# Optimization experiments

Hardware: AMD Instinct MI355X
Metric: run time of the kernel (lower is better)

The kernel has to match this reference:

```python
import jax, jax.numpy as jnp
import numpy as np

B, N, H = 128, 512, 512
NEG_INF = -1e30


def setup_inputs() -> dict:
    key = jax.random.key(0)
    k1, k2, k3, k4 = jax.random.split(key, 4)
    code_feat = jax.random.normal(k1, (B, N, H), dtype=jnp.float32)
    node_mask = jax.random.randint(k2, (B, N), 0, 2, dtype=jnp.int32)
    node_mask = node_mask.at[:, 0].set(1)  # ensure >=1 valid node per sample
    scale = 1.0 / np.sqrt(H)
    W_sa = jax.random.normal(k3, (H, H), dtype=jnp.float32) * scale
    b_sa = jnp.zeros((H,), dtype=jnp.float32)
    w_sc = jax.random.normal(k4, (H,), dtype=jnp.float32) * scale
    b_sc = jnp.zeros((), dtype=jnp.float32)
    return {"code_feat": code_feat, "node_mask": node_mask,
            "W_sa": W_sa, "b_sa": b_sa, "w_sc": w_sc, "b_sc": b_sc}


def reference(code_feat, node_mask, W_sa, b_sa, w_sc, b_sc):
    # code_sa_tanh = self_atten_scalar(tanh(self_atten(code_feat)))  -> [B, N]
    h = jnp.tanh(jnp.einsum('bnh,hk->bnk', code_feat, W_sa) + b_sa)
    scores = jnp.einsum('bnk,k->bn', h, w_sc) + b_sc  # [B, N]
    valid = node_mask.astype(bool)
    # masked_select + softmax over selected nodes == masked softmax; invalid
    # positions get weight 0, so the weighted sum over all nodes matches the
    # original per-sample bmm over the ragged selection exactly.
    scores = jnp.where(valid, scores, NEG_INF)
    attn = jax.nn.softmax(scores, axis=1)  # [B, N]
    pooled = jnp.einsum('bn,bnh->bh', attn, code_feat)  # [B, H]
    return jnp.tanh(pooled)
```

## Files before the change

### kernel.cpp

```cpp
#include <hip/hip_runtime.h>

#define NEG_INF (-1e30f)

typedef __bf16 bf16x8 __attribute__((ext_vector_type(8)));
typedef float  f32x4  __attribute__((ext_vector_type(4)));
typedef unsigned short ushort;

__device__ __forceinline__ float fast_tanhf(float x) {
    return 1.0f - 2.0f / (1.0f + __expf(2.0f * x));
}

__device__ __forceinline__ ushort f2bf(float f) {
    union { float f; unsigned u; } v; v.f = f;
    unsigned r = v.u + 0x7fffu + ((v.u >> 16) & 1u);
    return (ushort)(r >> 16);
}

__device__ __forceinline__ void gload_lds16(const void* gsrc, void* ldsdst) {
    __builtin_amdgcn_global_load_lds(
        (const __attribute__((address_space(1))) unsigned int*)gsrc,
        (__attribute__((address_space(3))) unsigned int*)ldsdst, 16, 0, 0);
}

__global__ void convw_kernel(const float* __restrict__ W, ushort* __restrict__ Wt) {
    int i = blockIdx.x * 256 + threadIdx.x;
    int h = i >> 9, c = i & 511;
    Wt[c * 512 + h] = f2bf(W[i]);
}

__global__ __launch_bounds__(256) void gemm_scores_kernel(
    const float* __restrict__ feat, const ushort* __restrict__ Wt,
    const float* __restrict__ b_sa, const float* __restrict__ w_sc,
    float* __restrict__ sp) {

    __shared__ ushort Alds[128 * 40];
    __shared__ ushort Blds[128 * 32];
    __shared__ float  redE[4][64];

    const int tid  = threadIdx.x;
    const int by   = blockIdx.x;
    const int m0   = blockIdx.y * 128;
    const int n0   = by * 128;
    const int lane = tid & 63;
    const int wv   = tid >> 6;
    const int wm   = wv >> 1, wn = wv & 1;
    const int lr   = lane & 15;
    const int kg   = lane >> 4;
    const int lk   = kg * 8;

    const int arow = tid >> 1;
    const int aseg = (tid & 1) * 16;
    const float* agp = feat + (size_t)(m0 + arow) * 512 + aseg;

    f32x4 acc[4][4];
#pragma unroll
    for (int a = 0; a < 4; ++a)
#pragma unroll
        for (int b = 0; b < 4; ++b) acc[a][b] = (f32x4){0.f, 0.f, 0.f, 0.f};

    const int o1 = tid + 256;
    const ushort* bg0 = Wt + (size_t)(n0 + (tid >> 2)) * 512 + (tid & 3) * 8;
    const ushort* bg1 = Wt + (size_t)(n0 + (o1 >> 2)) * 512 + (o1 & 3) * 8;

    for (int k0 = 0; k0 < 512; k0 += 32) {
        const float4 v0 = *reinterpret_cast<const float4*>(agp + k0);
        const float4 v1 = *reinterpret_cast<const float4*>(agp + k0 + 4);
        const float4 v2 = *reinterpret_cast<const float4*>(agp + k0 + 8);
        const float4 v3 = *reinterpret_cast<const float4*>(agp + k0 + 12);

        __syncthreads();

        gload_lds16(bg0 + k0, (char*)Blds + wv * 1024);
        gload_lds16(bg1 + k0, (char*)Blds + 4096 + wv * 1024);

        bf16x8 h0, h1;
        h0[0] = (__bf16)v0.x; h0[1] = (__bf16)v0.y; h0[2] = (__bf16)v0.z; h0[3] = (__bf16)v0.w;
        h0[4] = (__bf16)v1.x; h0[5] = (__bf16)v1.y; h0[6] = (__bf16)v1.z; h0[7] = (__bf16)v1.w;
        h1[0] = (__bf16)v2.x; h1[1] = (__bf16)v2.y; h1[2] = (__bf16)v2.z; h1[3] = (__bf16)v2.w;
        h1[4] = (__bf16)v3.x; h1[5] = (__bf16)v3.y; h1[6] = (__bf16)v3.z; h1[7] = (__bf16)v3.w;
        *reinterpret_cast<bf16x8*>(&Alds[arow * 40 + aseg]) = h0;
        *reinterpret_cast<bf16x8*>(&Alds[arow * 40 + aseg + 8]) = h1;

        __syncthreads();

        bf16x8 af[4], bfv[4];
#pragma unroll
        for (int a = 0; a < 4; ++a)
            af[a] = *reinterpret_cast<const bf16x8*>(
                &Alds[(wm * 64 + a * 16 + lr) * 40 + lk]);
#pragma unroll
        for (int b = 0; b < 4; ++b)
            bfv[b] = *reinterpret_cast<const bf16x8*>(&Blds[(wn * 64 + b * 16 + lr) * 32 + lk]);
#pragma unroll
        for (int a = 0; a < 4; ++a)
#pragma unroll
            for (int b = 0; b < 4; ++b)
                acc[a][b] = __builtin_amdgcn_mfma_f32_16x16x32_bf16(
                    af[a], bfv[b], acc[a][b], 0, 0, 0);
    }

    float rsum[4][4];
#pragma unroll
    for (int a = 0; a < 4; ++a)
#pragma unroll
        for (int r = 0; r < 4; ++r) rsum[a][r] = 0.0f;

#pragma unroll
    for (int b = 0; b < 4; ++b) {
        int col = n0 + wn * 64 + b * 16 + lr;
        float wsc = w_sc[col];
        float bsa = b_sa[col];
#pragma unroll
        for (int a = 0; a < 4; ++a)
#pragma unroll
            for (int r = 0; r < 4; ++r)
                rsum[a][r] += fast_tanhf(acc[a][b][r] + bsa) * wsc;
    }
#pragma unroll
    for (int a = 0; a < 4; ++a)
#pragma unroll
        for (int r = 0; r < 4; ++r) {
            float v = rsum[a][r];
            v += __shfl_xor(v, 1);
            v += __shfl_xor(v, 2);
            v += __shfl_xor(v, 4);
            v += __shfl_xor(v, 8);
            rsum[a][r] = v;
        }
    if (lr == 0) {
#pragma unroll
        for (int a = 0; a < 4; ++a)
#pragma unroll
            for (int r = 0; r < 4; ++r)
                redE[wv][a * 16 + kg * 4 + r] = rsum[a][r];
    }
    __syncthreads();
    if (tid < 128) {
        int wmo = tid >> 6, r64 = tid & 63;
        sp[(size_t)by * 65536 + m0 + tid] = redE[wmo * 2][r64] + redE[wmo * 2 + 1][r64];
    }
}

__global__ void softmax_kernel(const float* __restrict__ sp, const float* __restrict__ b_sc,
                               const int* __restrict__ mask, float* __restrict__ probs) {
    int b = blockIdx.x, t = threadIdx.x;
    int i0 = b * 512 + t, i1 = i0 + 256;
    float s0 = sp[i0] + sp[65536 + i0] + sp[131072 + i0] + sp[196608 + i0] + b_sc[0];
    float s1 = sp[i1] + sp[65536 + i1] + sp[131072 + i1] + sp[196608 + i1] + b_sc[0];
    if (!mask[i0]) s0 = NEG_INF;
    if (!mask[i1]) s1 = NEG_INF;
    float m = fmaxf(s0, s1);
#pragma unroll
    for (int o = 1; o < 64; o <<= 1) m = fmaxf(m, __shfl_xor(m, o));
    __shared__ float red[4];
    if ((t & 63) == 0) red[t >> 6] = m;
    __syncthreads();
    m = fmaxf(fmaxf(red[0], red[1]), fmaxf(red[2], red[3]));
    float e0 = __expf(s0 - m), e1 = __expf(s1 - m);
    float z = e0 + e1;
#pragma unroll
    for (int o = 1; o < 64; o <<= 1) z += __shfl_xor(z, o);
    __syncthreads();
    if ((t & 63) == 0) red[t >> 6] = z;
    __syncthreads();
    float inv = 1.0f / (red[0] + red[1] + red[2] + red[3]);
    probs[i0] = e0 * inv;
    probs[i1] = e1 * inv;
}

__global__ void pool_kernel(const float* __restrict__ feat,
                            const float* __restrict__ probs,
                            float* __restrict__ part) {
    int b = blockIdx.x, c = blockIdx.y, t = threadIdx.x;
    __shared__ float pl[128];
    __shared__ float red2[2][512];
    if (t < 128) pl[t] = probs[b * 512 + c * 128 + t];
    __syncthreads();
    int col4 = (t & 127) * 4;
    int stripe = t >> 7;
    const float* fb = feat + ((size_t)(b * 512 + c * 128 + stripe * 64)) * 512 + col4;
    float4 a4 = {0.f, 0.f, 0.f, 0.f};
#pragma unroll 8
    for (int n = 0; n < 64; ++n) {
        float p = pl[stripe * 64 + n];
        const float4 f4 = *reinterpret_cast<const float4*>(fb + (size_t)n * 512);
        a4.x = fmaf(p, f4.x, a4.x);
        a4.y = fmaf(p, f4.y, a4.y);
        a4.z = fmaf(p, f4.z, a4.z);
        a4.w = fmaf(p, f4.w, a4.w);
    }
    *reinterpret_cast<float4*>(&red2[stripe][col4]) = a4;
    __syncthreads();
    float x0 = red2[0][t] + red2[1][t];
    float x1 = red2[0][t + 256] + red2[1][t + 256];
    part[(size_t)c * 65536 + b * 512 + t]       = x0;
    part[(size_t)c * 65536 + b * 512 + t + 256] = x1;
}

__global__ void finish_kernel(const float* __restrict__ part, float* __restrict__ out) {
    int i = blockIdx.x * 256 + threadIdx.x;
    float s = part[i] + part[65536 + i] + part[131072 + i] + part[196608 + i];
    out[i] = fast_tanhf(s);
}

extern "C" void kernel_launch(void* const* d_in, const int* in_sizes, int n_in,
                              void* d_out, int out_size, void* d_ws, size_t ws_size,
                              hipStream_t stream) {
    const float* feat = (const float*)d_in[0];
    const int*   mask = (const int*)d_in[1];
    const float* W_sa = (const float*)d_in[2];
    const float* b_sa = (const float*)d_in[3];
    const float* w_sc = (const float*)d_in[4];
    const float* b_sc = (const float*)d_in[5];
    float* out = (float*)d_out;

    char* ws = (char*)d_ws;
    ushort* Wt    = (ushort*)ws;
    float*  sp    = (float*)(ws + (512 << 10));
    float*  probs = (float*)(ws + (512 << 10) + (1024 << 10));
    float*  part  = (float*)(ws + (512 << 10) + (1280 << 10));

    hipLaunchKernelGGL(convw_kernel, dim3(1024), dim3(256), 0, stream, W_sa, Wt);
    hipLaunchKernelGGL(gemm_scores_kernel, dim3(4, 512), dim3(256), 0, stream,
                       feat, Wt, b_sa, w_sc, sp);
    hipLaunchKernelGGL(softmax_kernel, dim3(128), dim3(256), 0, stream,
                       sp, b_sc, mask, probs);
    hipLaunchKernelGGL(pool_kernel, dim3(128, 4), dim3(256), 0, stream, feat, probs, part);
    hipLaunchKernelGGL(finish_kernel, dim3(256), dim3(256), 0, stream, part, out);
}
```

Measured before the change: 118.2 us.

## Double-buffer GEMM LDS tiles, swizzle block order, use MFMA-friendly LDS layout

The scores GEMM now keeps two LDS buffers for the A and B tiles and prefetches the next k-slice from global memory while MFMAs run on the current one, so each iteration needs one barrier instead of two. The grid is flattened and remapped so that the four column blocks sharing a row tile, and groups of row tiles, are scheduled close together, which should improve L2 reuse of the feature rows. The LDS layout is changed to a 16-row blocked arrangement matching the MFMA fragment reads, replacing the padded row-major layout. The cost is double the LDS footprint and more registers held live for the prefetched data.

```diff
diff --git a/kernel.cpp b/kernel.cpp
--- a/kernel.cpp
+++ b/kernel.cpp
@@ -33,24 +33,35 @@
     const float* __restrict__ b_sa, const float* __restrict__ w_sc,
     float* __restrict__ sp) {
 
-    __shared__ ushort Alds[128 * 40];
-    __shared__ ushort Blds[128 * 32];
+    __shared__ ushort Alds[2][4096];
+    __shared__ ushort Blds[2][4096];
     __shared__ float  redE[4][64];
 
     const int tid  = threadIdx.x;
-    const int by   = blockIdx.x;
-    const int m0   = blockIdx.y * 128;
+    const int id   = blockIdx.x;
+    const int g    = id & 7;
+    const int c8   = id >> 3;
+    const int my   = g * 64 + (c8 >> 2);
+    const int by   = c8 & 3;
+    const int m0   = my * 128;
     const int n0   = by * 128;
+
     const int lane = tid & 63;
     const int wv   = tid >> 6;
     const int wm   = wv >> 1, wn = wv & 1;
     const int lr   = lane & 15;
     const int kg   = lane >> 4;
-    const int lk   = kg * 8;
 
     const int arow = tid >> 1;
     const int aseg = (tid & 1) * 16;
     const float* agp = feat + (size_t)(m0 + arow) * 512 + aseg;
+    const int wA = (arow >> 4) * 512 + (aseg >> 3) * 128 + (arow & 15) * 8;
+
+    const ushort* bg0 = Wt + (size_t)(n0 + (0 * 4 + wv) * 16 + lr) * 512 + kg * 8;
+    const ushort* bg1 = Wt + (size_t)(n0 + (1 * 4 + wv) * 16 + lr) * 512 + kg * 8;
+
+    const int aBase = wm * 2048 + kg * 128 + lr * 8;
+    const int bBase = wn * 2048 + kg * 128 + lr * 8;
 
     f32x4 acc[4][4];
 #pragma unroll
@@ -58,45 +69,61 @@
 #pragma unroll
         for (int b = 0; b < 4; ++b) acc[a][b] = (f32x4){0.f, 0.f, 0.f, 0.f};
 
-    const int o1 = tid + 256;
-    const ushort* bg0 = Wt + (size_t)(n0 + (tid >> 2)) * 512 + (tid & 3) * 8;
-    const ushort* bg1 = Wt + (size_t)(n0 + (o1 >> 2)) * 512 + (o1 & 3) * 8;
-
+    float4 p0 = *reinterpret_cast<const float4*>(agp + 0);
+    float4 p1 = *reinterpret_cast<const float4*>(agp + 4);
+    float4 p2 = *reinterpret_cast<const float4*>(agp + 8);
+    float4 p3 = *reinterpret_cast<const float4*>(agp + 12);
+    gload_lds16(bg0, (char*)Blds[0] + wv * 1024);
+    gload_lds16(bg1, (char*)Blds[0] + 4096 + wv * 1024);
+    {
+        bf16x8 h0, h1;
+        h0[0] = (__bf16)p0.x; h0[1] = (__bf16)p0.y; h0[2] = (__bf16)p0.z; h0[3] = (__bf16)p0.w;
+        h0[4] = (__bf16)p1.x; h0[5] = (__bf16)p1.y; h0[6] = (__bf16)p1.z; h0[7] = (__bf16)p1.w;
+        h1[0] = (__bf16)p2.x; h1[1] = (__bf16)p2.y; h1[2] = (__bf16)p2.z; h1[3] = (__bf16)p2.w;
+        h1[4] = (__bf16)p3.x; h1[5] = (__bf16)p3.y; h1[6] = (__bf16)p3.z; h1[7] = (__bf16)p3.w;
+        *reinterpret_cast<bf16x8*>(&Alds[0][wA])       = h0;
+        *reinterpret_cast<bf16x8*>(&Alds[0][wA + 128]) = h1;
+    }
+    p0 = *reinterpret_cast<const float4*>(agp + 32);
+    p1 = *reinterpret_cast<const float4*>(agp + 36);
+    p2 = *reinterpret_cast<const float4*>(agp + 40);
+    p3 = *reinterpret_cast<const float4*>(agp + 44);
+    __syncthreads();
+
+    int p = 0;
     for (int k0 = 0; k0 < 512; k0 += 32) {
-        const float4 v0 = *reinterpret_cast<const float4*>(agp + k0);
-        const float4 v1 = *reinterpret_cast<const float4*>(agp + k0 + 4);
-        const float4 v2 = *reinterpret_cast<const float4*>(agp + k0 + 8);
-        const float4 v3 = *reinterpret_cast<const float4*>(agp + k0 + 12);
-
-        __syncthreads();
-
-        gload_lds16(bg0 + k0, (char*)Blds + wv * 1024);
-        gload_lds16(bg1 + k0, (char*)Blds + 4096 + wv * 1024);
-
-        bf16x8 h0, h1;
-        h0[0] = (__bf16)v0.x; h0[1] = (__bf16)v0.y; h0[2] = (__bf16)v0.z; h0[3] = (__bf16)v0.w;
-        h0[4] = (__bf16)v1.x; h0[5] = (__bf16)v1.y; h0[6] = (__bf16)v1.z; h0[7] = (__bf16)v1.w;
-        h1[0] = (__bf16)v2.x; h1[1] = (__bf16)v2.y; h1[2] = (__bf16)v2.z; h1[3] = (__bf16)v2.w;
-        h1[4] = (__bf16)v3.x; h1[5] = (__bf16)v3.y; h1[6] = (__bf16)v3.z; h1[7] = (__bf16)v3.w;
-        *reinterpret_cast<bf16x8*>(&Alds[arow * 40 + aseg]) = h0;
-        *reinterpret_cast<bf16x8*>(&Alds[arow * 40 + aseg + 8]) = h1;
-
-        __syncthreads();
-
+        if (k0 < 480) {
+            bf16x8 h0, h1;
+            h0[0] = (__bf16)p0.x; h0[1] = (__bf16)p0.y; h0[2] = (__bf16)p0.z; h0[3] = (__bf16)p0.w;
+            h0[4] = (__bf16)p1.x; h0[5] = (__bf16)p1.y; h0[6] = (__bf16)p1.z; h0[7] = (__bf16)p1.w;
+            h1[0] = (__bf16)p2.x; h1[1] = (__bf16)p2.y; h1[2] = (__bf16)p2.z; h1[3] = (__bf16)p2.w;
+            h1[4] = (__bf16)p3.x; h1[5] = (__bf16)p3.y; h1[6] = (__bf16)p3.z; h1[7] = (__bf16)p3.w;
+            *reinterpret_cast<bf16x8*>(&Alds[p ^ 1][wA])       = h0;
+            *reinterpret_cast<bf16x8*>(&Alds[p ^ 1][wA + 128]) = h1;
+            gload_lds16(bg0 + k0 + 32, (char*)Blds[p ^ 1] + wv * 1024);
+            gload_lds16(bg1 + k0 + 32, (char*)Blds[p ^ 1] + 4096 + wv * 1024);
+            if (k0 < 448) {
+                p0 = *reinterpret_cast<const float4*>(agp + k0 + 64);
+                p1 = *reinterpret_cast<const float4*>(agp + k0 + 68);
+                p2 = *reinterpret_cast<const float4*>(agp + k0 + 72);
+                p3 = *reinterpret_cast<const float4*>(agp + k0 + 76);
+            }
+        }
         bf16x8 af[4], bfv[4];
 #pragma unroll
         for (int a = 0; a < 4; ++a)
-            af[a] = *reinterpret_cast<const bf16x8*>(
-                &Alds[(wm * 64 + a * 16 + lr) * 40 + lk]);
+            af[a] = *reinterpret_cast<const bf16x8*>(&Alds[p][aBase + a * 512]);
 #pragma unroll
         for (int b = 0; b < 4; ++b)
-            bfv[b] = *reinterpret_cast<const bf16x8*>(&Blds[(wn * 64 + b * 16 + lr) * 32 + lk]);
+            bfv[b] = *reinterpret_cast<const bf16x8*>(&Blds[p][bBase + b * 512]);
 #pragma unroll
         for (int a = 0; a < 4; ++a)
 #pragma unroll
             for (int b = 0; b < 4; ++b)
                 acc[a][b] = __builtin_amdgcn_mfma_f32_16x16x32_bf16(
                     af[a], bfv[b], acc[a][b], 0, 0, 0);
+        __syncthreads();
+        p ^= 1;
     }
 
     float rsum[4][4];
@@ -221,7 +248,7 @@
     float*  part  = (float*)(ws + (512 << 10) + (1280 << 10));
 
     hipLaunchKernelGGL(convw_kernel, dim3(1024), dim3(256), 0, stream, W_sa, Wt);
-    hipLaunchKernelGGL(gemm_scores_kernel, dim3(4, 512), dim3(256), 0, stream,
+    hipLaunchKernelGGL(gemm_scores_kernel, dim3(2048), dim3(256), 0, stream,
                        feat, Wt, b_sa, w_sc, sp);
     hipLaunchKernelGGL(softmax_kernel, dim3(128), dim3(256), 0, stream,
                        sp, b_sc, mask, probs);
```

Measured after the change: 107.4 us. 9.1% less time.

## Restructure score GEMM: A fragments direct from global, B staged in LDS

Applied to the files above, without the earlier changes.

The score GEMM is rebuilt around 512-thread blocks covering 256 rows by 128 columns. Each wave loads its own 32 rows of the fp32 features straight from global memory into registers and converts them to bf16, so the A tile no longer goes through LDS. The weight half-tile (256 K values) is staged in LDS with only two barrier passes instead of one pair per 32-wide K step. Block IDs are swizzled into groups of 8 for cache locality, the cross-wave LDS reduction is replaced by direct per-wave stores, and tanh uses a hardware reciprocal. The risks are uncoalesced per-lane A loads, higher register pressure from the 2x8 accumulators, and 64KB of LDS limiting occupancy.

```diff
diff --git a/kernel.cpp b/kernel.cpp
--- a/kernel.cpp
+++ b/kernel.cpp
@@ -7,7 +7,8 @@
 typedef unsigned short ushort;
 
 __device__ __forceinline__ float fast_tanhf(float x) {
-    return 1.0f - 2.0f / (1.0f + __expf(2.0f * x));
+    float e = __expf(2.0f * x);
+    return 1.0f - 2.0f * __builtin_amdgcn_rcpf(1.0f + e);
 }
 
 __device__ __forceinline__ ushort f2bf(float f) {
@@ -28,116 +29,102 @@
     Wt[c * 512 + h] = f2bf(W[i]);
 }
 
-__global__ __launch_bounds__(256) void gemm_scores_kernel(
+__global__ __launch_bounds__(512) void gemm_scores_kernel(
     const float* __restrict__ feat, const ushort* __restrict__ Wt,
     const float* __restrict__ b_sa, const float* __restrict__ w_sc,
     float* __restrict__ sp) {
 
-    __shared__ ushort Alds[128 * 40];
-    __shared__ ushort Blds[128 * 32];
-    __shared__ float  redE[4][64];
+    __shared__ ushort Blds[32768];
 
     const int tid  = threadIdx.x;
-    const int by   = blockIdx.x;
-    const int m0   = blockIdx.y * 128;
-    const int n0   = by * 128;
+    const int wv   = tid >> 6;
     const int lane = tid & 63;
-    const int wv   = tid >> 6;
-    const int wm   = wv >> 1, wn = wv & 1;
     const int lr   = lane & 15;
     const int kg   = lane >> 4;
-    const int lk   = kg * 8;
-
-    const int arow = tid >> 1;
-    const int aseg = (tid & 1) * 16;
-    const float* agp = feat + (size_t)(m0 + arow) * 512 + aseg;
-
-    f32x4 acc[4][4];
-#pragma unroll
-    for (int a = 0; a < 4; ++a)
-#pragma unroll
-        for (int b = 0; b < 4; ++b) acc[a][b] = (f32x4){0.f, 0.f, 0.f, 0.f};
-
-    const int o1 = tid + 256;
-    const ushort* bg0 = Wt + (size_t)(n0 + (tid >> 2)) * 512 + (tid & 3) * 8;
-    const ushort* bg1 = Wt + (size_t)(n0 + (o1 >> 2)) * 512 + (o1 & 3) * 8;
-
-    for (int k0 = 0; k0 < 512; k0 += 32) {
-        const float4 v0 = *reinterpret_cast<const float4*>(agp + k0);
-        const float4 v1 = *reinterpret_cast<const float4*>(agp + k0 + 4);
-        const float4 v2 = *reinterpret_cast<const float4*>(agp + k0 + 8);
-        const float4 v3 = *reinterpret_cast<const float4*>(agp + k0 + 12);
-
+
+    const int id   = blockIdx.x;
+    const int g    = id & 7;
+    const int loc  = id >> 3;
+    const int msuper = g * 32 + (loc >> 2);
+    const int by   = loc & 3;
+    const int m0   = msuper * 256;
+    const int n0   = by * 128;
+    const int mw   = m0 + wv * 32;
+
+    const float*  ag0  = feat + (size_t)(mw + lr) * 512 + kg * 8;
+    const float*  ag1  = ag0 + 16 * 512;
+    const ushort* bsrc = Wt + (size_t)(n0 + wv * 16 + lr) * 512 + kg * 8;
+
+    f32x4 acc[2][8];
+#pragma unroll
+    for (int gr = 0; gr < 2; ++gr)
+#pragma unroll
+        for (int cf = 0; cf < 8; ++cf) acc[gr][cf] = (f32x4){0.f, 0.f, 0.f, 0.f};
+
+    for (int pass = 0; pass < 2; ++pass) {
+        if (pass) __syncthreads();
+#pragma unroll
+        for (int r = 0; r < 8; ++r)
+            gload_lds16(bsrc + pass * 256 + r * 32,
+                        (char*)Blds + r * 8192 + wv * 1024);
         __syncthreads();
 
-        gload_lds16(bg0 + k0, (char*)Blds + wv * 1024);
-        gload_lds16(bg1 + k0, (char*)Blds + 4096 + wv * 1024);
-
-        bf16x8 h0, h1;
-        h0[0] = (__bf16)v0.x; h0[1] = (__bf16)v0.y; h0[2] = (__bf16)v0.z; h0[3] = (__bf16)v0.w;
-        h0[4] = (__bf16)v1.x; h0[5] = (__bf16)v1.y; h0[6] = (__bf16)v1.z; h0[7] = (__bf16)v1.w;
-        h1[0] = (__bf16)v2.x; h1[1] = (__bf16)v2.y; h1[2] = (__bf16)v2.z; h1[3] = (__bf16)v2.w;
-        h1[4] = (__bf16)v3.x; h1[5] = (__bf16)v3.y; h1[6] = (__bf16)v3.z; h1[7] = (__bf16)v3.w;
-        *reinterpret_cast<bf16x8*>(&Alds[arow * 40 + aseg]) = h0;
-        *reinterpret_cast<bf16x8*>(&Alds[arow * 40 + aseg + 8]) = h1;
-
-        __syncthreads();
-
-        bf16x8 af[4], bfv[4];
-#pragma unroll
-        for (int a = 0; a < 4; ++a)
-            af[a] = *reinterpret_cast<const bf16x8*>(
-                &Alds[(wm * 64 + a * 16 + lr) * 40 + lk]);
-#pragma unroll
-        for (int b = 0; b < 4; ++b)
-            bfv[b] = *reinterpret_cast<const bf16x8*>(&Blds[(wn * 64 + b * 16 + lr) * 32 + lk]);
-#pragma unroll
-        for (int a = 0; a < 4; ++a)
-#pragma unroll
-            for (int b = 0; b < 4; ++b)
-                acc[a][b] = __builtin_amdgcn_mfma_f32_16x16x32_bf16(
-                    af[a], bfv[b], acc[a][b], 0, 0, 0);
-    }
-
-    float rsum[4][4];
-#pragma unroll
-    for (int a = 0; a < 4; ++a)
-#pragma unroll
-        for (int r = 0; r < 4; ++r) rsum[a][r] = 0.0f;
-
-#pragma unroll
-    for (int b = 0; b < 4; ++b) {
-        int col = n0 + wn * 64 + b * 16 + lr;
-        float wsc = w_sc[col];
-        float bsa = b_sa[col];
-#pragma unroll
-        for (int a = 0; a < 4; ++a)
+#pragma unroll
+        for (int kl = 0; kl < 8; ++kl) {
+            const int kgl = pass * 256 + kl * 32;
+            const float4 q0 = *reinterpret_cast<const float4*>(ag0 + kgl);
+            const float4 q1 = *reinterpret_cast<const float4*>(ag0 + kgl + 4);
+            const float4 q2 = *reinterpret_cast<const float4*>(ag1 + kgl);
+            const float4 q3 = *reinterpret_cast<const float4*>(ag1 + kgl + 4);
+            bf16x8 a0, a1;
+            a0[0] = (__bf16)q0.x; a0[1] = (__bf16)q0.y; a0[2] = (__bf16)q0.z; a0[3] = (__bf16)q0.w;
+            a0[4] = (__bf16)q1.x; a0[5] = (__bf16)q1.y; a0[6] = (__bf16)q1.z; a0[7] = (__bf16)q1.w;
+            a1[0] = (__bf16)q2.x; a1[1] = (__bf16)q2.y; a1[2] = (__bf16)q2.z; a1[3] = (__bf16)q2.w;
+            a1[4] = (__bf16)q3.x; a1[5] = (__bf16)q3.y; a1[6] = (__bf16)q3.z; a1[7] = (__bf16)q3.w;
+#pragma unroll
+            for (int cf = 0; cf < 8; ++cf) {
+                const bf16x8 bf = *reinterpret_cast<const bf16x8*>(
+                    (const char*)Blds + kl * 8192 + cf * 1024 + kg * 256 + lr * 16);
+                acc[0][cf] = __builtin_amdgcn_mfma_f32_16x16x32_bf16(a0, bf, acc[0][cf], 0, 0, 0);
+                acc[1][cf] = __builtin_amdgcn_mfma_f32_16x16x32_bf16(a1, bf, acc[1][cf], 0, 0, 0);
+            }
+        }
+    }
+
+    float rs[2][4];
+#pragma unroll
+    for (int gr = 0; gr < 2; ++gr)
+#pragma unroll
+        for (int r = 0; r < 4; ++r) rs[gr][r] = 0.0f;
+
+#pragma unroll
+    for (int cf = 0; cf < 8; ++cf) {
+        const int col = n0 + cf * 16 + lr;
+        const float w = w_sc[col];
+        const float b = b_sa[col];
+#pragma unroll
+        for (int gr = 0; gr < 2; ++gr)
 #pragma unroll
             for (int r = 0; r < 4; ++r)
-                rsum[a][r] += fast_tanhf(acc[a][b][r] + bsa) * wsc;
-    }
-#pragma unroll
-    for (int a = 0; a < 4; ++a)
+                rs[gr][r] += fast_tanhf(acc[gr][cf][r] + b) * w;
+    }
+#pragma unroll
+    for (int gr = 0; gr < 2; ++gr)
 #pragma unroll
         for (int r = 0; r < 4; ++r) {
-            float v = rsum[a][r];
+            float v = rs[gr][r];
             v += __shfl_xor(v, 1);
             v += __shfl_xor(v, 2);
             v += __shfl_xor(v, 4);
             v += __shfl_xor(v, 8);
-            rsum[a][r] = v;
+            rs[gr][r] = v;
         }
     if (lr == 0) {
 #pragma unroll
-        for (int a = 0; a < 4; ++a)
+        for (int gr = 0; gr < 2; ++gr)
 #pragma unroll
             for (int r = 0; r < 4; ++r)
-                redE[wv][a * 16 + kg * 4 + r] = rsum[a][r];
-    }
-    __syncthreads();
-    if (tid < 128) {
-        int wmo = tid >> 6, r64 = tid & 63;
-        sp[(size_t)by * 65536 + m0 + tid] = redE[wmo * 2][r64] + redE[wmo * 2 + 1][r64];
+                sp[(size_t)by * 65536 + mw + gr * 16 + kg * 4 + r] = rs[gr][r];
     }
 }
 
@@ -221,7 +208,7 @@
     float*  part  = (float*)(ws + (512 << 10) + (1280 << 10));
 
     hipLaunchKernelGGL(convw_kernel, dim3(1024), dim3(256), 0, stream, W_sa, Wt);
-    hipLaunchKernelGGL(gemm_scores_kernel, dim3(4, 512), dim3(256), 0, stream,
+    hipLaunchKernelGGL(gemm_scores_kernel, dim3(1024), dim3(512), 0, stream,
                        feat, Wt, b_sa, w_sc, sp);
     hipLaunchKernelGGL(softmax_kernel, dim3(128), dim3(256), 0, stream,
                        sp, b_sc, mask, probs);
```

Measured after the change: 114.3 us. -3.3%, faster.
